# Kernel optimization log

Measured on AMD Instinct MI355X. Metric: run time of the kernel, lower is better.

## Reference

```python
import jax, jax.numpy as jnp
import numpy as np

N = 50000        # nodes
E = 800000       # edges (avg degree 16)
C_IN = 128
H = 256          # hidden_channels
C_OUT = 128
DEPTH = 4
K = 2            # k_hops -> K+1 = 3 TAGConv weight matrices
L = DEPTH - 1    # residual layers after layer-0 conv
EPS = 1e-5
SLOPE = 0.01     # LeakyReLU default negative slope


def setup_inputs() -> dict:
    key = jax.random.key(0)
    ks = iter(jax.random.split(key, 24))
    s = 0.02
    x = jax.random.normal(next(ks), (N, C_IN), dtype=jnp.float32)
    edge_index = jax.random.randint(next(ks), (2, E), 0, N, dtype=jnp.int64)
    edge_weight = jax.random.uniform(next(ks), (E,), dtype=jnp.float32)
    return {
        'x': x,
        'edge_index': edge_index,
        'edge_weight': edge_weight,
        'W_emb': jax.random.normal(next(ks), (C_IN, H)) * s,
        'b_emb': jnp.zeros((H,), jnp.float32),
        'conv0_W': jax.random.normal(next(ks), (K + 1, H, H)) * s,
        'conv0_b': jnp.zeros((H,), jnp.float32),
        'norm_g': jnp.ones((L, H), jnp.float32),
        'norm_b': jnp.zeros((L, H), jnp.float32),
        'conv_W': jax.random.normal(next(ks), (L, K + 1, H, H)) * s,
        'conv_b': jnp.zeros((L, H), jnp.float32),
        'mlp_W1': jax.random.normal(next(ks), (L, H, 4 * H)) * s,
        'mlp_b1': jnp.zeros((L, 4 * H), jnp.float32),
        'mlp_g': jnp.ones((L, 4 * H), jnp.float32),
        'mlp_bb': jnp.zeros((L, 4 * H), jnp.float32),
        'mlp_W2': jax.random.normal(next(ks), (L, 4 * H, H)) * s,
        'mlp_b2': jnp.zeros((L, H), jnp.float32),
        'W_out': jax.random.normal(next(ks), (H, C_OUT)) * s,
        'b_out': jnp.zeros((C_OUT,), jnp.float32),
    }


def _bn(h, g, b):
    # BatchNorm1d over node dim (training-mode batch statistics)
    m = h.mean(axis=0)
    v = h.var(axis=0)
    return g * (h - m) * jax.lax.rsqrt(v + EPS) + b


def _tagconv(h, src, dst, ew, Ws, b):
    # TAGConv (normalize=False, no self loops): sum_k (A^k h) W_k + b
    out = h @ Ws[0]
    p = h
    for k in range(1, Ws.shape[0]):
        msg = p[src] * ew[:, None]                      # [E, H] gather
        p = jax.ops.segment_sum(msg, dst, num_segments=h.shape[0])
        out = out + p @ Ws[k]
    return out + b


def reference(x, edge_index, edge_weight, W_emb, b_emb, conv0_W, conv0_b,
              norm_g, norm_b, conv_W, conv_b, mlp_W1, mlp_b1, mlp_g, mlp_bb,
              mlp_W2, mlp_b2, W_out, b_out):
    src, dst = edge_index[0], edge_index[1]
    h = x @ W_emb + b_emb                               # x_embed (t=None)
    h = _tagconv(h, src, dst, edge_weight, conv0_W, conv0_b)  # layer-0 conv only
    for l in range(norm_g.shape[0]):                    # res+ blocks
        z = jax.nn.leaky_relu(_bn(h, norm_g[l], norm_b[l]), SLOPE)
        z = _tagconv(z, src, dst, edge_weight, conv_W[l], conv_b[l])
        # pyg MLP [H, 4H, H]: Linear -> BN -> act -> Linear (plain last)
        z = jax.nn.leaky_relu(_bn(z @ mlp_W1[l] + mlp_b1[l], mlp_g[l], mlp_bb[l]), SLOPE)
        z = z @ mlp_W2[l] + mlp_b2[l]
        h = h + z                                       # residual (res=Identity)
    return h @ W_out + b_out
```

## Files before the change

### kernel.cpp

```cpp
#include <hip/hip_runtime.h>

#define HDIM 256
#define EPSV 1e-5f
#define SLOPEV 0.01f

typedef __bf16 bf16;
typedef bf16  bf16x8 __attribute__((ext_vector_type(8)));
typedef bf16  bf16x4 __attribute__((ext_vector_type(4)));
typedef float f32x4  __attribute__((ext_vector_type(4)));

#define GLD16(g, l) __builtin_amdgcn_global_load_lds( \
    (const __attribute__((address_space(1))) void*)(g), \
    (__attribute__((address_space(3))) void*)(l), 16, 0, 0)

template<bool STORE_BF16, bool STATS, bool FUSE_A>
__global__ __launch_bounds__(256, 5)
void gemm_bt_k(const bf16* A0, const bf16* A1, const bf16* A2, const bf16* A3,
               int nseg, int segK,
               const bf16* __restrict__ Wt,
               const float* __restrict__ bias, const bf16* __restrict__ addb,
               void* out0, void* out1, void* out2, void* out3, int ldo,
               int n_store, float* part, int n_stats,
               const float* __restrict__ fcoef, int fuse_nseg, int ncoef)
{
    constexpr int SMEMSZ = FUSE_A ? 32768 : 24576;
    __shared__ char smem[SMEMSZ];

    const int tid = threadIdx.x;
    const int wave = tid >> 6, lane = tid & 63;
    const int quad = lane >> 4, l16 = lane & 15;
    const int waveM = (wave >> 1) * 32, waveN = (wave & 1) * 64;

    int bid = blockIdx.y * gridDim.x + blockIdx.x;
    const int nwg = gridDim.x * gridDim.y;
    if ((nwg & 7) == 0) {
        const int cpx = nwg >> 3;
        bid = (bid & 7) * cpx + (bid >> 3);
    }
    const int bx = bid % gridDim.x, by = bid / gridDim.x;
    const int bm = by * 64, bn = bx * 128;
    const int K = nseg * segK;

    const bf16* segs[4] = {A0, A1, A2, A3};
    const int srow = tid >> 2;
    const int skof = (tid & 3) * 8;

    f32x4 acc[2][4] = {};

    const int T = K >> 5;

    auto stageA = [&](int s, int kt, int b) {
        const bf16* gA = segs[s] + (size_t)(bm + srow) * segK + kt + skof;
        GLD16(gA, smem + b * 4096 + wave * 1024);
    };
    auto stageB = [&](int s, int kt, int b) {
        const bf16* gB = Wt + (size_t)(bn + srow) * K + s * segK + kt + skof;
        char* lB = smem + 8192 + b * 8192 + wave * 1024;
        GLD16(gB,                  lB);
        GLD16(gB + (size_t)64 * K, lB + 4096);
    };

    if (FUSE_A) {
        float* aT = (float*)(smem + 24576);
        float* bT = aT + 1024;
        for (int i = tid; i < ncoef; i += 256) {
            aT[i] = fcoef[i];
            bT[i] = fcoef[ncoef + i];
        }
    }
    stageA(0, 0, 0);
    stageB(0, 0, 0);
    __syncthreads();

    int s = 0, kt = 0;
    for (int t = 0; t < T; ++t) {
        int s2 = s, kt2 = kt + 32;
        if (kt2 == segK) { s2++; kt2 = 0; }
        if (t + 1 < T) {
            stageA(s2, kt2, (t + 1) & 1);
            stageB(s2, kt2, (t + 1) & 1);
        }

        const bf16* pa = (const bf16*)(smem + (t & 1) * 4096)
                         + (waveM + l16) * 32 + quad * 8;
        const bf16* pb = (const bf16*)(smem + 8192 + (t & 1) * 8192)
                         + (waveN + l16) * 32 + quad * 8;
        bf16x8 a0 = *(const bf16x8*)(pa);
        bf16x8 a1 = *(const bf16x8*)(pa + 16 * 32);
        bf16x8 b0 = *(const bf16x8*)(pb);
        bf16x8 b1 = *(const bf16x8*)(pb + 16 * 32);
        bf16x8 b2 = *(const bf16x8*)(pb + 32 * 32);
        bf16x8 b3 = *(const bf16x8*)(pb + 48 * 32);

        if (FUSE_A && s < fuse_nseg) {
            const float* aT = (const float*)(smem + 24576);
            const float* bT = aT + 1024;
            int kb = s * segK + kt + quad * 8;
            float av[8], dv[8];
            *(float4*)(av)     = *(const float4*)(aT + kb);
            *(float4*)(av + 4) = *(const float4*)(aT + kb + 4);
            *(float4*)(dv)     = *(const float4*)(bT + kb);
            *(float4*)(dv + 4) = *(const float4*)(bT + kb + 4);
#pragma unroll
            for (int u = 0; u < 8; ++u) {
                float f0 = fmaf((float)a0[u], av[u], dv[u]);
                f0 = f0 > 0.f ? f0 : SLOPEV * f0;
                a0[u] = (bf16)f0;
                float f1 = fmaf((float)a1[u], av[u], dv[u]);
                f1 = f1 > 0.f ? f1 : SLOPEV * f1;
                a1[u] = (bf16)f1;
            }
        }

        acc[0][0] = __builtin_amdgcn_mfma_f32_16x16x32_bf16(a0, b0, acc[0][0], 0, 0, 0);
        acc[0][1] = __builtin_amdgcn_mfma_f32_16x16x32_bf16(a0, b1, acc[0][1], 0, 0, 0);
        acc[0][2] = __builtin_amdgcn_mfma_f32_16x16x32_bf16(a0, b2, acc[0][2], 0, 0, 0);
        acc[0][3] = __builtin_amdgcn_mfma_f32_16x16x32_bf16(a0, b3, acc[0][3], 0, 0, 0);
        acc[1][0] = __builtin_amdgcn_mfma_f32_16x16x32_bf16(a1, b0, acc[1][0], 0, 0, 0);
        acc[1][1] = __builtin_amdgcn_mfma_f32_16x16x32_bf16(a1, b1, acc[1][1], 0, 0, 0);
        acc[1][2] = __builtin_amdgcn_mfma_f32_16x16x32_bf16(a1, b2, acc[1][2], 0, 0, 0);
        acc[1][3] = __builtin_amdgcn_mfma_f32_16x16x32_bf16(a1, b3, acc[1][3], 0, 0, 0);

        __syncthreads();
        s = s2; kt = kt2;
    }

    float bv[4];
#pragma unroll
    for (int j = 0; j < 4; ++j)
        bv[j] = bias ? bias[bn + waveN + j * 16 + l16] : 0.f;
#pragma unroll
    for (int i = 0; i < 2; ++i)
#pragma unroll
        for (int j = 0; j < 4; ++j)
#pragma unroll
            for (int r = 0; r < 4; ++r)
                acc[i][j][r] += bv[j];

    void* outs[4] = {out0, out1, out2, out3};

    if (STORE_BF16) {
        char* stg = smem + wave * 4608;
        float s8[8] = {}, q8[8] = {};
        const int rsel = lane >> 3, csel = lane & 7;
#pragma unroll
        for (int i = 0; i < 2; ++i)
#pragma unroll
            for (int j = 0; j < 4; ++j)
#pragma unroll
                for (int r = 0; r < 4; ++r)
                    *(bf16*)(stg + ((i * 16 + quad * 4 + r) * 72 + j * 16 + l16) * 2)
                        = (bf16)acc[i][j][r];
#pragma unroll
        for (int rr = 0; rr < 4; ++rr) {
            int rl = rsel + rr * 8;
            bf16x8 v = *(const bf16x8*)(stg + (rl * 72 + csel * 8) * 2);
            int rowg = bm + waveM + rl;
            int colg = bn + waveN + csel * 8;
            int cseg = colg >> 8, cloc = colg & 255;
            size_t idx = (size_t)rowg * ldo + cloc;
            float f[8];
#pragma unroll
            for (int u = 0; u < 8; ++u) f[u] = (float)v[u];
            if (addb) {
                bf16x8 o = *(const bf16x8*)(addb + idx);
#pragma unroll
                for (int u = 0; u < 8; ++u) f[u] += (float)o[u];
            }
            bf16x8 w;
#pragma unroll
            for (int u = 0; u < 8; ++u) w[u] = (bf16)f[u];
            if (rowg < n_store) *(bf16x8*)((bf16*)outs[cseg] + idx) = w;
            if (STATS && rowg < n_stats) {
#pragma unroll
                for (int u = 0; u < 8; ++u) { s8[u] += f[u]; q8[u] += f[u] * f[u]; }
            }
        }
        if (STATS) {
#pragma unroll
            for (int m = 8; m <= 32; m <<= 1)
#pragma unroll
                for (int u = 0; u < 8; ++u) {
                    s8[u] += __shfl_xor(s8[u], m, 64);
                    q8[u] += __shfl_xor(q8[u], m, 64);
                }
            float* Ls = (float*)(smem + 18432);
            float* Lq = Ls + 256;
            if (rsel == 0) {
#pragma unroll
                for (int u = 0; u < 8; ++u) {
                    Ls[wave * 64 + csel * 8 + u] = s8[u];
                    Lq[wave * 64 + csel * 8 + u] = q8[u];
                }
            }
            __syncthreads();
            if (tid < 128) {
                int hi = tid >> 6, c6 = tid & 63;
                float sv = Ls[hi * 64 + c6] + Ls[(hi + 2) * 64 + c6];
                float qv = Lq[hi * 64 + c6] + Lq[(hi + 2) * 64 + c6];
                int Mtot = gridDim.x * 128;
                int colg = bn + tid;
                part[(size_t)by * Mtot + colg] = sv;
                part[(size_t)(gridDim.y + by) * Mtot + colg] = qv;
            }
        }
    } else {
#pragma unroll
        for (int i = 0; i < 2; ++i)
#pragma unroll
            for (int j = 0; j < 4; ++j) {
                int colg = bn + waveN + j * 16 + l16;
                int cseg = colg >> 8, cloc = colg & 255;
#pragma unroll
                for (int r = 0; r < 4; ++r) {
                    int rowg = bm + waveM + i * 16 + quad * 4 + r;
                    if (rowg < n_store)
                        ((float*)outs[cseg])[(size_t)rowg * ldo + cloc] = acc[i][j][r];
                }
            }
    }
}

__global__ __launch_bounds__(256)
void finalize_k(const float* __restrict__ part, int GY, int M,
                const float* __restrict__ g, const float* __restrict__ bb,
                float* __restrict__ coef, float invn)
{
    const int c = blockIdx.x;
    const int t = threadIdx.x;
    float s = 0.f, q = 0.f;
    const float* ps = part + c;
    const float* pq = part + (size_t)GY * M + c;
    for (int i = t; i < GY; i += 256) {
        s += ps[(size_t)i * M];
        q += pq[(size_t)i * M];
    }
#pragma unroll
    for (int m = 1; m <= 32; m <<= 1) {
        s += __shfl_xor(s, m, 64);
        q += __shfl_xor(q, m, 64);
    }
    __shared__ float Ls[4], Lq[4];
    const int w = t >> 6, l = t & 63;
    if (l == 0) { Ls[w] = s; Lq[w] = q; }
    __syncthreads();
    if (t == 0) {
        s = Ls[0] + Ls[1] + Ls[2] + Ls[3];
        q = Lq[0] + Lq[1] + Lq[2] + Lq[3];
        float mean = s * invn;
        float var  = q * invn - mean * mean;
        float a = g[c] * rsqrtf(var + EPSV);
        coef[c]     = a;
        coef[M + c] = bb[c] - mean * a;
    }
}

__global__ __launch_bounds__(256)
void transpose_cvt_k(const float* __restrict__ src, bf16* __restrict__ dst,
                     int Kseg, int M, int G)
{
    __shared__ float t[32][33];
    const int z = blockIdx.z;
    src += (size_t)z * Kseg * M;
    const int ldd = G * Kseg;
    dst += (size_t)(z / G) * M * ldd + (size_t)(z % G) * Kseg;
    const int tM = blockIdx.x * 32, tK = blockIdx.y * 32;
    const int tx = threadIdx.x & 31, ty = threadIdx.x >> 5;
#pragma unroll
    for (int r = 0; r < 4; ++r)
        t[ty + r * 8][tx] = src[(size_t)(tK + ty + r * 8) * M + tM + tx];
    __syncthreads();
#pragma unroll
    for (int r = 0; r < 4; ++r)
        dst[(size_t)(tM + ty + r * 8) * ldd + tK + tx] = (bf16)t[tx][ty + r * 8];
}

__global__ __launch_bounds__(256)
void cvt_bf_k(const float* __restrict__ src, bf16* __restrict__ dst, long n4)
{
    long i = (long)blockIdx.x * blockDim.x + threadIdx.x;
    if (i >= n4) return;
    float4 v = ((const float4*)src)[i];
    bf16x4 o; o[0] = (bf16)v.x; o[1] = (bf16)v.y; o[2] = (bf16)v.z; o[3] = (bf16)v.w;
    ((bf16x4*)dst)[i] = o;
}

__global__ __launch_bounds__(256)
void deg_k(const int* __restrict__ dst, int* __restrict__ deg, int E)
{
    int e = blockIdx.x * blockDim.x + threadIdx.x;
    if (e < E) atomicAdd(&deg[dst[e]], 1);
}

__global__ __launch_bounds__(256)
void blocksum_k(const int* __restrict__ deg, int* __restrict__ bsum, int N)
{
    int i = blockIdx.x * 256 + threadIdx.x;
    int v = (i < N) ? deg[i] : 0;
#pragma unroll
    for (int m = 1; m <= 32; m <<= 1) v += __shfl_xor(v, m, 64);
    __shared__ int Ls[4];
    if ((threadIdx.x & 63) == 0) Ls[threadIdx.x >> 6] = v;
    __syncthreads();
    if (threadIdx.x == 0) bsum[blockIdx.x] = Ls[0] + Ls[1] + Ls[2] + Ls[3];
}

__global__ __launch_bounds__(256)
void topscan_k(const int* __restrict__ bsum, int* __restrict__ boff, int nb)
{
    __shared__ int s[256];
    int t = threadIdx.x;
    int v = (t < nb) ? bsum[t] : 0;
    s[t] = v;
    __syncthreads();
    for (int off = 1; off < 256; off <<= 1) {
        int u = (t >= off) ? s[t - off] : 0;
        __syncthreads();
        s[t] += u;
        __syncthreads();
    }
    if (t < nb) boff[t] = s[t] - v;
}

__global__ __launch_bounds__(256)
void scatterscan_k(int* __restrict__ deg_wp, const int* __restrict__ boff,
                   int* __restrict__ rowptr, int N)
{
    __shared__ int s[256];
    int t = threadIdx.x;
    int i = blockIdx.x * 256 + t;
    int v = (i < N) ? deg_wp[i] : 0;
    s[t] = v;
    __syncthreads();
    for (int off = 1; off < 256; off <<= 1) {
        int u = (t >= off) ? s[t - off] : 0;
        __syncthreads();
        s[t] += u;
        __syncthreads();
    }
    if (i < N) {
        int incl = s[t] + boff[blockIdx.x];
        rowptr[i + 1] = incl;
        deg_wp[i] = incl - v;
        if (i == 0) rowptr[0] = 0;
    }
}

__global__ __launch_bounds__(256)
void reorder_k(const int* __restrict__ src, const int* __restrict__ dst,
               const float* __restrict__ ew, int* __restrict__ wp,
               int* __restrict__ col, float* __restrict__ wgt, int E)
{
    int e = blockIdx.x * blockDim.x + threadIdx.x;
    if (e >= E) return;
    int d = dst[e];
    int pos = atomicAdd(&wp[d], 1);
    col[pos] = src[e];
    wgt[pos] = ew[e];
}

template<bool FUSE>
__global__ __launch_bounds__(256)
void spmm_pull_k(const bf16* __restrict__ P, const int* __restrict__ rowptr,
                 const int* __restrict__ col, const float* __restrict__ wgt,
                 bf16* __restrict__ Q, int N, const float* __restrict__ coef)
{
    int node = blockIdx.x * 8 + (threadIdx.x >> 5);
    int l = threadIdx.x & 31;
    if (node >= N) return;
    float a8[8], b8[8];
    if (FUSE) {
#pragma unroll
        for (int u = 0; u < 8; ++u) {
            a8[u] = coef[l * 8 + u];
            b8[u] = coef[256 + l * 8 + u];
        }
    }
    auto tx = [&](float x, int u) {
        if (FUSE) {
            x = fmaf(x, a8[u], b8[u]);
            x = x > 0.f ? x : SLOPEV * x;
        }
        return x;
    };
    int e = rowptr[node], end = rowptr[node + 1];
    float acc[8] = {};
    for (; e + 3 < end; e += 4) {
        int   s0 = col[e],     s1 = col[e + 1], s2 = col[e + 2], s3 = col[e + 3];
        float w0 = wgt[e],     w1 = wgt[e + 1], w2 = wgt[e + 2], w3 = wgt[e + 3];
        bf16x8 v0 = *(const bf16x8*)(P + (size_t)s0 * HDIM + l * 8);
        bf16x8 v1 = *(const bf16x8*)(P + (size_t)s1 * HDIM + l * 8);
        bf16x8 v2 = *(const bf16x8*)(P + (size_t)s2 * HDIM + l * 8);
        bf16x8 v3 = *(const bf16x8*)(P + (size_t)s3 * HDIM + l * 8);
#pragma unroll
        for (int u = 0; u < 8; ++u)
            acc[u] += (tx((float)v0[u], u) * w0 + tx((float)v1[u], u) * w1)
                    + (tx((float)v2[u], u) * w2 + tx((float)v3[u], u) * w3);
    }
    for (; e + 1 < end; e += 2) {
        int   s0 = col[e], s1 = col[e + 1];
        float w0 = wgt[e], w1 = wgt[e + 1];
        bf16x8 v0 = *(const bf16x8*)(P + (size_t)s0 * HDIM + l * 8);
        bf16x8 v1 = *(const bf16x8*)(P + (size_t)s1 * HDIM + l * 8);
#pragma unroll
        for (int u = 0; u < 8; ++u)
            acc[u] += tx((float)v0[u], u) * w0 + tx((float)v1[u], u) * w1;
    }
    if (e < end) {
        int s0 = col[e]; float w0 = wgt[e];
        bf16x8 v0 = *(const bf16x8*)(P + (size_t)s0 * HDIM + l * 8);
#pragma unroll
        for (int u = 0; u < 8; ++u) acc[u] += tx((float)v0[u], u) * w0;
    }
    bf16x8 o;
#pragma unroll
    for (int u = 0; u < 8; ++u) o[u] = (bf16)acc[u];
    *(bf16x8*)(Q + (size_t)node * HDIM + l * 8) = o;
}

struct GemmArgs {
    const bf16 *A0, *A1, *A2, *A3; int nseg, segK;
    const bf16* Wt; const float* bias; const bf16* addb;
    void *o0, *o1, *o2, *o3; int ldo, M, n_store;
    float* part; int n_stats;
    const float* fuse; int fuse_nseg; int ncoef;
};

static void gemm(hipStream_t st, const GemmArgs& a, int GYr, bool store_bf16, bool stats)
{
    dim3 g(a.M / 128, GYr), b(256);
    if (a.fuse) {
        if (stats)
            gemm_bt_k<true, true, true><<<g, b, 0, st>>>(a.A0, a.A1, a.A2, a.A3,
                a.nseg, a.segK, a.Wt, a.bias, a.addb, a.o0, a.o1, a.o2, a.o3,
                a.ldo, a.n_store, a.part, a.n_stats, a.fuse, a.fuse_nseg, a.ncoef);
        else
            gemm_bt_k<true, false, true><<<g, b, 0, st>>>(a.A0, a.A1, a.A2, a.A3,
                a.nseg, a.segK, a.Wt, a.bias, a.addb, a.o0, a.o1, a.o2, a.o3,
                a.ldo, a.n_store, a.part, a.n_stats, a.fuse, a.fuse_nseg, a.ncoef);
    } else if (store_bf16) {
        if (stats)
            gemm_bt_k<true, true, false><<<g, b, 0, st>>>(a.A0, a.A1, a.A2, a.A3,
                a.nseg, a.segK, a.Wt, a.bias, a.addb, a.o0, a.o1, a.o2, a.o3,
                a.ldo, a.n_store, a.part, a.n_stats, nullptr, 0, 0);
        else
            gemm_bt_k<true, false, false><<<g, b, 0, st>>>(a.A0, a.A1, a.A2, a.A3,
                a.nseg, a.segK, a.Wt, a.bias, a.addb, a.o0, a.o1, a.o2, a.o3,
                a.ldo, a.n_store, a.part, a.n_stats, nullptr, 0, 0);
    } else {
        gemm_bt_k<false, false, false><<<g, b, 0, st>>>(a.A0, a.A1, a.A2, a.A3,
            a.nseg, a.segK, a.Wt, a.bias, a.addb, a.o0, a.o1, a.o2, a.o3,
            a.ldo, a.n_store, a.part, a.n_stats, nullptr, 0, 0);
    }
}

extern "C" void kernel_launch(void* const* d_in, const int* in_sizes, int n_in,
                              void* d_out, int out_size, void* d_ws, size_t ws_size,
                              hipStream_t stream)
{
    const float* x       = (const float*)d_in[0];
    const int*   ei      = (const int*)d_in[1];
    const float* ew      = (const float*)d_in[2];
    const float* W_emb   = (const float*)d_in[3];
    const float* b_emb   = (const float*)d_in[4];
    const float* conv0_W = (const float*)d_in[5];
    const float* conv0_b = (const float*)d_in[6];
    const float* norm_g  = (const float*)d_in[7];
    const float* norm_b  = (const float*)d_in[8];
    const float* conv_W  = (const float*)d_in[9];
    const float* conv_b  = (const float*)d_in[10];
    const float* mlp_W1  = (const float*)d_in[11];
    const float* mlp_b1  = (const float*)d_in[12];
    const float* mlp_g   = (const float*)d_in[13];
    const float* mlp_bb  = (const float*)d_in[14];
    const float* mlp_W2  = (const float*)d_in[15];
    const float* mlp_b2  = (const float*)d_in[16];
    const float* W_out   = (const float*)d_in[17];
    const float* b_out   = (const float*)d_in[18];

    const int N = in_sizes[0] / 128;
    const int E = in_sizes[2];
    const int* srcI = ei;
    const int* dstI = ei + E;
    const int N_pad = ((N + 127) / 128) * 128;
    const int GYr = N_pad / 64;
    const int NB = (N + 255) / 256;

    const size_t NHp = (size_t)N_pad * HDIM;
    bf16* xb = (bf16*)d_ws;
    bf16* hb = xb + (size_t)N_pad * 128;
    bf16* cb = hb + NHp;
    bf16* p1 = cb + NHp;
    bf16* p2 = p1 + NHp;
    bf16* e1 = p2 + NHp;
    bf16* e2 = e1 + NHp;
    bf16* wa = e2 + NHp;
    bf16* Wt_emb   = wa;
    bf16* Wt_conv0 = wa + 32768;
    bf16* Wt_conv  = wa + 229376;
    bf16* Wt_mlp1  = wa + 819200;
    bf16* Wt_mlp2  = wa + 1605632;
    bf16* Wt_out   = wa + 2392064;
    float* cf_h   = (float*)(wa + 2424832);
    float* cf_m   = cf_h + 512;
    float* partb  = cf_m + 2048;
    int*   rowptr = (int*)(partb + 2 * (size_t)GYr * 1024);
    int*   wp     = rowptr + (N + 1);
    int*   col    = wp + N;
    float* wgt    = (float*)(col + E);
    int*   bsum   = (int*)(wgt + E);
    int*   boff   = bsum + 256;

    const float invn = 1.0f / (float)N;
    dim3 pg((N + 7) / 8), pb(256);

    hipMemsetAsync(wp, 0, (size_t)N * 4, stream);
    deg_k<<<dim3((E + 255) / 256), dim3(256), 0, stream>>>(dstI, wp, E);
    blocksum_k<<<dim3(NB), dim3(256), 0, stream>>>(wp, bsum, N);
    topscan_k<<<dim3(1), dim3(256), 0, stream>>>(bsum, boff, NB);
    scatterscan_k<<<dim3(NB), dim3(256), 0, stream>>>(wp, boff, rowptr, N);
    reorder_k<<<dim3((E + 255) / 256), dim3(256), 0, stream>>>(srcI, dstI, ew, wp, col, wgt, E);

    cvt_bf_k<<<dim3((N * 32 + 255) / 256), dim3(256), 0, stream>>>(x, xb, (long)N * 32);
    transpose_cvt_k<<<dim3(8, 4, 1), dim3(256), 0, stream>>>(W_emb, Wt_emb, 128, 256, 1);
    transpose_cvt_k<<<dim3(8, 8, 3), dim3(256), 0, stream>>>(conv0_W, Wt_conv0, 256, 256, 3);
    transpose_cvt_k<<<dim3(8, 8, 9), dim3(256), 0, stream>>>(conv_W, Wt_conv, 256, 256, 3);
    transpose_cvt_k<<<dim3(32, 8, 3), dim3(256), 0, stream>>>(mlp_W1, Wt_mlp1, 256, 1024, 1);
    transpose_cvt_k<<<dim3(8, 32, 3), dim3(256), 0, stream>>>(mlp_W2, Wt_mlp2, 1024, 256, 1);
    transpose_cvt_k<<<dim3(4, 8, 1), dim3(256), 0, stream>>>(W_out, Wt_out, 256, 128, 1);

    {
        GemmArgs a{xb, xb, xb, xb, 1, 128, Wt_emb, b_emb, nullptr,
                   cb, cb, cb, cb, HDIM, 256, N_pad, nullptr, 0, nullptr, 0, 0};
        gemm(stream, a, GYr, true, false);
    }

    spmm_pull_k<false><<<pg, pb, 0, stream>>>(cb, rowptr, col, wgt, p1, N, nullptr);
    spmm_pull_k<false><<<pg, pb, 0, stream>>>(p1, rowptr, col, wgt, p2, N, nullptr);
    {
        GemmArgs a{cb, p1, p2, p2, 3, 256, Wt_conv0, conv0_b, nullptr,
                   hb, hb, hb, hb, HDIM, 256, N_pad, partb, N, nullptr, 0, 0};
        gemm(stream, a, GYr, true, true);
    }
    finalize_k<<<dim3(256), dim3(256), 0, stream>>>(partb, GYr, 256, norm_g, norm_b, cf_h, invn);

    for (int l = 0; l < 3; ++l) {
        spmm_pull_k<true><<<pg, pb, 0, stream>>>(hb, rowptr, col, wgt, p1, N, cf_h);
        spmm_pull_k<false><<<pg, pb, 0, stream>>>(p1, rowptr, col, wgt, p2, N, nullptr);
        {
            GemmArgs a{hb, p1, p2, p2, 3, 256, Wt_conv + (size_t)l * 196608,
                       conv_b + l * 256, nullptr, cb, cb, cb, cb, HDIM, 256, N_pad,
                       nullptr, 0, cf_h, 1, 256};
            gemm(stream, a, GYr, true, false);
        }

        {
            GemmArgs a{cb, cb, cb, cb, 1, 256, Wt_mlp1 + (size_t)l * 262144,
                       mlp_b1 + (size_t)l * 1024, nullptr, p1, p2, e1, e2, HDIM, 1024,
                       N_pad, partb, N, nullptr, 0, 0};
            gemm(stream, a, GYr, true, true);
        }
        finalize_k<<<dim3(1024), dim3(256), 0, stream>>>(partb, GYr, 1024,
                                                         mlp_g + (size_t)l * 1024,
                                                         mlp_bb + (size_t)l * 1024, cf_m, invn);

        {
            GemmArgs a{p1, p2, e1, e2, 4, 256, Wt_mlp2 + (size_t)l * 262144,
                       mlp_b2 + l * 256, hb, hb, hb, hb, hb, HDIM, 256, N_pad,
                       (l < 2) ? partb : nullptr, N, cf_m, 4, 1024};
            gemm(stream, a, GYr, true, l < 2);
        }
        if (l < 2)
            finalize_k<<<dim3(256), dim3(256), 0, stream>>>(partb, GYr, 256,
                                                            norm_g + (l + 1) * 256,
                                                            norm_b + (l + 1) * 256, cf_h, invn);
    }

    {
        GemmArgs a{hb, hb, hb, hb, 1, 256, Wt_out, b_out, nullptr,
                   d_out, d_out, d_out, d_out, 128, 128, N, nullptr, 0, nullptr, 0, 0};
        gemm(stream, a, GYr, false, false);
    }
}
```

Before: 1.381 ms.

## Shrink fused GEMM LDS, raise occupancy bound, unroll SpMM gather by eight

```diff
diff --git a/kernel.cpp b/kernel.cpp
--- a/kernel.cpp
+++ b/kernel.cpp
@@ -14,7 +14,7 @@
     (__attribute__((address_space(3))) void*)(l), 16, 0, 0)
 
 template<bool STORE_BF16, bool STATS, bool FUSE_A>
-__global__ __launch_bounds__(256, 5)
+__global__ __launch_bounds__(256, FUSE_A ? 5 : 6)
 void gemm_bt_k(const bf16* A0, const bf16* A1, const bf16* A2, const bf16* A3,
                int nseg, int segK,
                const bf16* __restrict__ Wt,
@@ -23,7 +23,7 @@
                int n_store, float* part, int n_stats,
                const float* __restrict__ fcoef, int fuse_nseg, int ncoef)
 {
-    constexpr int SMEMSZ = FUSE_A ? 32768 : 24576;
+    constexpr int SMEMSZ = FUSE_A ? 26624 : 24576;
     __shared__ char smem[SMEMSZ];
 
     const int tid = threadIdx.x;
@@ -60,20 +60,23 @@
         GLD16(gB + (size_t)64 * K, lB + 4096);
     };
 
-    if (FUSE_A) {
-        float* aT = (float*)(smem + 24576);
-        float* bT = aT + 1024;
-        for (int i = tid; i < ncoef; i += 256) {
-            aT[i] = fcoef[i];
-            bT[i] = fcoef[ncoef + i];
-        }
-    }
     stageA(0, 0, 0);
     stageB(0, 0, 0);
     __syncthreads();
 
     int s = 0, kt = 0;
+    int curSeg = -1;
     for (int t = 0; t < T; ++t) {
+        if (FUSE_A && s < fuse_nseg && s != curSeg) {
+            if (tid < segK) {
+                float* aT = (float*)(smem + 24576);
+                aT[tid]        = fcoef[s * segK + tid];
+                aT[256 + tid]  = fcoef[ncoef + s * segK + tid];
+            }
+            __syncthreads();
+            curSeg = s;
+        }
+
         int s2 = s, kt2 = kt + 32;
         if (kt2 == segK) { s2++; kt2 = 0; }
         if (t + 1 < T) {
@@ -94,8 +97,8 @@
 
         if (FUSE_A && s < fuse_nseg) {
             const float* aT = (const float*)(smem + 24576);
-            const float* bT = aT + 1024;
-            int kb = s * segK + kt + quad * 8;
+            const float* bT = aT + 256;
+            int kb = kt + quad * 8;
             float av[8], dv[8];
             *(float4*)(av)     = *(const float4*)(aT + kb);
             *(float4*)(av + 4) = *(const float4*)(aT + kb + 4);
@@ -104,11 +107,9 @@
 #pragma unroll
             for (int u = 0; u < 8; ++u) {
                 float f0 = fmaf((float)a0[u], av[u], dv[u]);
-                f0 = f0 > 0.f ? f0 : SLOPEV * f0;
-                a0[u] = (bf16)f0;
+                a0[u] = (bf16)fmaxf(f0, SLOPEV * f0);
                 float f1 = fmaf((float)a1[u], av[u], dv[u]);
-                f1 = f1 > 0.f ? f1 : SLOPEV * f1;
-                a1[u] = (bf16)f1;
+                a1[u] = (bf16)fmaxf(f1, SLOPEV * f1);
             }
         }
 
@@ -379,12 +380,26 @@
     auto tx = [&](float x, int u) {
         if (FUSE) {
             x = fmaf(x, a8[u], b8[u]);
-            x = x > 0.f ? x : SLOPEV * x;
+            x = fmaxf(x, SLOPEV * x);
         }
         return x;
     };
     int e = rowptr[node], end = rowptr[node + 1];
     float acc[8] = {};
+    for (; e + 7 < end; e += 8) {
+        int   sx[8]; float wx[8];
+#pragma unroll
+        for (int k = 0; k < 8; ++k) { sx[k] = col[e + k]; wx[k] = wgt[e + k]; }
+        bf16x8 v[8];
+#pragma unroll
+        for (int k = 0; k < 8; ++k)
+            v[k] = *(const bf16x8*)(P + (size_t)sx[k] * HDIM + l * 8);
+#pragma unroll
+        for (int k = 0; k < 8; ++k)
+#pragma unroll
+            for (int u = 0; u < 8; ++u)
+                acc[u] += tx((float)v[k][u], u) * wx[k];
+    }
     for (; e + 3 < end; e += 4) {
         int   s0 = col[e],     s1 = col[e + 1], s2 = col[e + 2], s3 = col[e + 3];
         float w0 = wgt[e],     w1 = wgt[e + 1], w2 = wgt[e + 2], w3 = wgt[e + 3];
```

Result: no change. 1.369 ms (-0.9%).
